# Optimization experiments

Hardware: AMD Instinct MI355X
Metric: run time of the kernel (lower is better)

Reference implementation:

```python
import jax, jax.numpy as jnp
import numpy as np

NH = 8          # attention heads
TOP_K = 2       # MoE top-k


def _ln(x, g, b, eps=1e-5):
    mu = x.mean(-1, keepdims=True)
    var = ((x - mu) ** 2).mean(-1, keepdims=True)
    return (x - mu) * jax.lax.rsqrt(var + eps) * g + b


def setup_inputs() -> dict:
    key = jax.random.key(0)
    ks = jax.random.split(key, 12)
    B, C, S, P, E, HID, NEXP, NCLS = 128, 3, 224, 16, 256, 1024, 6, 1000
    N = (S // P) ** 2
    def n(k, shape, scale=0.02):
        return scale * jax.random.normal(k, shape, jnp.float32)
    return dict(
        x=jax.random.normal(ks[0], (B, C, S, S), jnp.float32),
        conv_w=n(ks[1], (E, C, P, P)),
        conv_b=jnp.zeros((E,), jnp.float32),
        pos_embed=n(ks[2], (1, N, E)),
        ln1_g=jnp.ones((E,), jnp.float32), ln1_b=jnp.zeros((E,), jnp.float32),
        wqkv=n(ks[3], (3 * E, E)), bqkv=jnp.zeros((3 * E,), jnp.float32),
        wo=n(ks[4], (E, E)), bo=jnp.zeros((E,), jnp.float32),
        router_w=n(ks[5], (NEXP, E)), router_b=jnp.zeros((NEXP,), jnp.float32),
        w1=n(ks[6], (NEXP, E, HID)), b1=jnp.zeros((NEXP, HID), jnp.float32),
        w2=n(ks[7], (NEXP, HID, E)), b2=jnp.zeros((NEXP, E), jnp.float32),
        ln2_g=jnp.ones((E,), jnp.float32), ln2_b=jnp.zeros((E,), jnp.float32),
        head_w=n(ks[8], (NCLS, E)), head_b=jnp.zeros((NCLS,), jnp.float32),
    )


def reference(x, conv_w, conv_b, pos_embed, ln1_g, ln1_b, wqkv, bqkv, wo, bo,
              router_w, router_b, w1, b1, w2, b2, ln2_g, ln2_b, head_w, head_b):
    B, C, S, _ = x.shape
    E, _, P, _ = conv_w.shape
    G = S // P
    N = G * G
    hd = E // NH
    # --- patch embedding: strided conv == per-patch linear ---
    xr = x.reshape(B, C, G, P, G, P)
    tok = jnp.einsum('bchpwq,ecpq->bhwe', xr, conv_w).reshape(B, N, E) + conv_b
    tok = tok + pos_embed  # dropout is identity in eval
    # --- self-attention block (pre-norm, residual) ---
    xn = _ln(tok, ln1_g, ln1_b)
    qkv = xn @ wqkv.T + bqkv
    q, k, v = jnp.split(qkv, 3, axis=-1)
    q = q.reshape(B, N, NH, hd)
    k = k.reshape(B, N, NH, hd)
    v = v.reshape(B, N, NH, hd)
    scores = jnp.einsum('bqhd,bkhd->bhqk', q, k) / np.float32(np.sqrt(hd))
    attn = jax.nn.softmax(scores, axis=-1)
    ao = jnp.einsum('bhqk,bkhd->bqhd', attn, v).reshape(B, N, E)
    x1 = tok + ao @ wo.T + bo
    # --- MoE (top-k routing, eval: no noise) ---
    T = B * N
    flat = x1.reshape(T, E)
    probs = jax.nn.softmax(flat @ router_w.T + router_b, axis=-1)
    topw, topi = jax.lax.top_k(probs, TOP_K)  # [T,k]
    out = jnp.zeros_like(flat)
    n_experts = router_w.shape[0]
    for e in range(n_experts):  # fixed small expert loop
        gate = jnp.sum(jnp.where(topi == e, topw, 0.0), axis=-1)  # [T], 0 if unrouted
        h = jax.nn.gelu(flat @ w1[e] + b1[e], approximate=False)
        y = h @ w2[e] + b2[e]
        out = out + gate[:, None] * y
    # --- final norm, pool, head ---
    x2 = _ln(out.reshape(B, N, E), ln2_g, ln2_b)
    pooled = x2.mean(axis=1)
    return pooled @ head_w.T + head_b
```

## Files before the change

### kernel.cpp

```cpp
#include <hip/hip_runtime.h>
#include <hip/hip_bf16.h>

typedef unsigned short u16;
typedef short short8 __attribute__((ext_vector_type(8)));
typedef short short4v __attribute__((ext_vector_type(4)));
typedef float f32x4 __attribute__((ext_vector_type(4)));

#define T_TOK 25088
#define NTOK 196
#define SWZ(r, c) ((((((c) >> 3) ^ ((r) & 7)) << 3)) | ((c) & 7))
#define SWZ4(r, c) ((((((c) >> 2) & 16) | ((((c) >> 2) ^ (r)) & 15)) << 2) | ((c) & 3))

__device__ __forceinline__ u16 bfbits(float v) {
  __hip_bfloat16 h = __float2bfloat16(v);
  return *reinterpret_cast<u16*>(&h);
}
__device__ __forceinline__ float b2f(u16 u) {
  __hip_bfloat16 h = *reinterpret_cast<__hip_bfloat16*>(&u);
  return __bfloat162float(h);
}
__device__ __forceinline__ void fsplit(float v, u16& hi, u16& lo) {
  hi = bfbits(v);
  lo = bfbits(v - b2f(hi));
}

template<int EPI, bool SPLITA>
__global__ __launch_bounds__(256) void gemm_bs(
    const u16* __restrict__ A, const u16* __restrict__ Al,
    const u16* __restrict__ Bh, const u16* __restrict__ Bl,
    int M, int N, int K,
    const float* __restrict__ bias, const float* __restrict__ extra,
    float* __restrict__ outf, u16* __restrict__ obh)
{
  __shared__ u16 As[128][40];
  __shared__ u16 Asl[SPLITA ? 128 : 1][40];
  __shared__ u16 Bsh[128][40], Bsl[128][40];
  const int tid = threadIdx.x;
  const int lane = tid & 63, wave = tid >> 6;
  const int wm = wave >> 1, wn = wave & 1;
  const int row0 = blockIdx.x * 128, col0 = blockIdx.y * 128;

  const int r0 = tid >> 2, r1 = r0 + 64, co = (tid & 3) * 8;
  const int ar0 = row0 + r0, ar1 = row0 + r1;

  f32x4 acc[4][4];
  const f32x4 zero = {0.f, 0.f, 0.f, 0.f};
#pragma unroll
  for (int i = 0; i < 4; ++i)
#pragma unroll
    for (int j = 0; j < 4; ++j) acc[i][j] = zero;

  const int rsel = lane & 15, ksel = (lane >> 4) * 8;

  short8 ra, rl, rb0, rb1, rc0, rc1;
  auto issue = [&](int k0) {
    ra = *(const short8*)(A + (size_t)ar0 * K + k0 + co);
    rl = *(const short8*)(A + (size_t)ar1 * K + k0 + co);
    rb0 = *(const short8*)(Bh + (size_t)(col0 + r0) * K + k0 + co);
    rb1 = *(const short8*)(Bh + (size_t)(col0 + r1) * K + k0 + co);
    rc0 = *(const short8*)(Bl + (size_t)(col0 + r0) * K + k0 + co);
    rc1 = *(const short8*)(Bl + (size_t)(col0 + r1) * K + k0 + co);
  };
  short8 sa, sl;
  auto issueS = [&](int k0) {
    if constexpr (SPLITA) {
      sa = *(const short8*)(Al + (size_t)ar0 * K + k0 + co);
      sl = *(const short8*)(Al + (size_t)ar1 * K + k0 + co);
    }
  };
  auto commit = [&]() {
    *(short8*)&As[r0][co] = ra;
    *(short8*)&As[r1][co] = rl;
    if constexpr (SPLITA) {
      *(short8*)&Asl[r0][co] = sa;
      *(short8*)&Asl[r1][co] = sl;
    }
    *(short8*)&Bsh[r0][co] = rb0;
    *(short8*)&Bsh[r1][co] = rb1;
    *(short8*)&Bsl[r0][co] = rc0;
    *(short8*)&Bsl[r1][co] = rc1;
  };

  issue(0);
  issueS(0);
  commit();
  __syncthreads();

  for (int k0 = 0;;) {
    const bool more = (k0 + 32 < K);
    if (more) { issue(k0 + 32); issueS(k0 + 32); }
    short8 af[4], al4[4], bh4[4], bl4[4];
#pragma unroll
    for (int i = 0; i < 4; ++i) {
      af[i] = *(const short8*)&As[wm * 64 + i * 16 + rsel][ksel];
      if constexpr (SPLITA) al4[i] = *(const short8*)&Asl[wm * 64 + i * 16 + rsel][ksel];
    }
#pragma unroll
    for (int j = 0; j < 4; ++j) {
      bh4[j] = *(const short8*)&Bsh[wn * 64 + j * 16 + rsel][ksel];
      bl4[j] = *(const short8*)&Bsl[wn * 64 + j * 16 + rsel][ksel];
    }
#pragma unroll
    for (int i = 0; i < 4; ++i)
#pragma unroll
      for (int j = 0; j < 4; ++j) {
        acc[i][j] = __builtin_amdgcn_mfma_f32_16x16x32_bf16(af[i], bh4[j], acc[i][j], 0, 0, 0);
        if constexpr (SPLITA)
          acc[i][j] = __builtin_amdgcn_mfma_f32_16x16x32_bf16(al4[i], bh4[j], acc[i][j], 0, 0, 0);
        acc[i][j] = __builtin_amdgcn_mfma_f32_16x16x32_bf16(af[i], bl4[j], acc[i][j], 0, 0, 0);
      }
    k0 += 32;
    if (!more) break;
    __syncthreads();
    commit();
    __syncthreads();
  }

#pragma unroll
  for (int i = 0; i < 4; ++i) {
#pragma unroll
    for (int j = 0; j < 4; ++j) {
#pragma unroll
      for (int r = 0; r < 4; ++r) {
        int grow = row0 + wm * 64 + i * 16 + (lane >> 4) * 4 + r;
        int gcol = col0 + wn * 64 + j * 16 + rsel;
        float v = acc[i][j][r] + bias[gcol];
        size_t oi = (size_t)grow * N + gcol;
        if constexpr (EPI == 1) {
          v += extra[(size_t)(grow % NTOK) * N + gcol];
          outf[oi] = v;
        } else if constexpr (EPI == 2) {
          v += extra[oi];
          outf[oi] = v;
          obh[oi] = bfbits(v);
        } else if constexpr (EPI == 5) {
          obh[oi] = bfbits(v);
        }
      }
    }
  }
}

__global__ __launch_bounds__(512, 4) void moe_fused(
    const u16* __restrict__ x1h,
    const u16* __restrict__ w1, const u16* __restrict__ w2,
    const float* __restrict__ b1, const float* __restrict__ b2,
    const float* __restrict__ gates,
    const int* __restrict__ idx_all, const int* __restrict__ cnt_all,
    const int* __restrict__ base_all,
    float* __restrict__ yslot)
{
  const int e = blockIdx.z;
  const int Meff = cnt_all[e];
  const int row0 = blockIdx.x * 64;
  if (row0 >= Meff) return;
  const int* gidx = idx_all + (size_t)e * T_TOK;
  const int hbase = base_all[e];
  const u16* W1 = w1 + (size_t)e * 262144;
  const u16* W2 = w2 + (size_t)e * 262144;
  const float* B1 = b1 + e * 1024;
  const float* B2 = b2 + e * 256;

  __shared__ u16 Xs[64][256];
  __shared__ u16 Hs[64][128];
  __shared__ u16 Ws[2 * 128 * 64];

  const int tid = threadIdx.x, lane = tid & 63, wn = tid >> 6;
  const int rsel = lane & 15, ksel = (lane >> 4) * 8;
  const f32x4 zero = {0.f, 0.f, 0.f, 0.f};

  const int w1r = tid >> 2, w1c = ((2 * tid) & 7) * 8;
  const int w2r = tid >> 1, w2c = ((4 * tid) & 7) * 8;

  short8 w1a = *(const short8*)(W1 + (size_t)w1r * 256 + w1c);
  short8 w1b = *(const short8*)(W1 + (size_t)w1r * 256 + w1c + 8);
  for (int ch = tid; ch < 2048; ch += 512) {
    int r = ch >> 5, c = (ch & 31) * 8;
    int arr = gidx[min(row0 + r, Meff - 1)];
    *(short8*)&Xs[r][SWZ(r, c)] = *(const short8*)(x1h + (size_t)arr * 256 + c);
  }

  f32x4 acc2[2][4];
#pragma unroll
  for (int i = 0; i < 2; ++i)
#pragma unroll
    for (int j = 0; j < 4; ++j) acc2[i][j] = zero;

  f32x4 acc1[4];

  auto ph1 = [&](int st, int buf) {
#pragma unroll
    for (int kk = 0; kk < 2; ++kk) {
      int wrow = wn * 16 + rsel;
      int wc = kk * 32 + ksel;
      short8 wf = *(const short8*)&Ws[buf * 8192 + wrow * 64 + SWZ(wrow, wc)];
      int kglob = st * 64 + kk * 32 + ksel;
#pragma unroll
      for (int tt = 0; tt < 4; ++tt) {
        int xrow = tt * 16 + rsel;
        short8 xf = *(const short8*)&Xs[xrow][SWZ(xrow, kglob)];
        acc1[tt] = __builtin_amdgcn_mfma_f32_16x16x32_bf16(wf, xf, acc1[tt], 0, 0, 0);
      }
    }
  };
  auto ph2 = [&](int st) {
#pragma unroll
    for (int kk = 0; kk < 2; ++kk) {
      int wc = kk * 32 + ksel;
      short8 wf[2];
#pragma unroll
      for (int ot = 0; ot < 2; ++ot) {
        int wrow = wn * 32 + ot * 16 + rsel;
        wf[ot] = *(const short8*)&Ws[wrow * 64 + SWZ(wrow, wc)];
      }
      int kc = st * 64 + kk * 32 + ksel;
#pragma unroll
      for (int tt = 0; tt < 4; ++tt) {
        int tok = tt * 16 + rsel;
        short4v lo = *(const short4v*)&Hs[tok][SWZ4(tok, kc)];
        short4v hi = *(const short4v*)&Hs[tok][SWZ4(tok, kc + 4)];
        short8 hf = {lo[0], lo[1], lo[2], lo[3], hi[0], hi[1], hi[2], hi[3]};
#pragma unroll
        for (int ot = 0; ot < 2; ++ot)
          acc2[ot][tt] = __builtin_amdgcn_mfma_f32_16x16x32_bf16(wf[ot], hf, acc2[ot][tt], 0, 0, 0);
      }
    }
  };

  for (int hc = 0; hc < 8; ++hc) {
    const u16* W1c = W1 + (size_t)hc * 128 * 256;
    const u16* W2c = W2 + hc * 128;
    short8 q0 = *(const short8*)(W2c + (size_t)w2r * 1024 + w2c);
    short8 q1 = *(const short8*)(W2c + (size_t)w2r * 1024 + w2c + 8);
    short8 q2 = *(const short8*)(W2c + (size_t)w2r * 1024 + w2c + 16);
    short8 q3 = *(const short8*)(W2c + (size_t)w2r * 1024 + w2c + 24);

#pragma unroll
    for (int i = 0; i < 4; ++i) acc1[i] = zero;

    *(short8*)&Ws[w1r * 64 + SWZ(w1r, w1c)] = w1a;
    *(short8*)&Ws[w1r * 64 + SWZ(w1r, w1c + 8)] = w1b;
    short8 p0 = *(const short8*)(W1c + (size_t)w1r * 256 + 64 + w1c);
    short8 p1 = *(const short8*)(W1c + (size_t)w1r * 256 + 64 + w1c + 8);
    __syncthreads();
    short8 s0 = *(const short8*)(W1c + (size_t)w1r * 256 + 128 + w1c);
    short8 s1 = *(const short8*)(W1c + (size_t)w1r * 256 + 128 + w1c + 8);
    ph1(0, 0);
    *(short8*)&Ws[8192 + w1r * 64 + SWZ(w1r, w1c)] = p0;
    *(short8*)&Ws[8192 + w1r * 64 + SWZ(w1r, w1c + 8)] = p1;
    __syncthreads();
    p0 = *(const short8*)(W1c + (size_t)w1r * 256 + 192 + w1c);
    p1 = *(const short8*)(W1c + (size_t)w1r * 256 + 192 + w1c + 8);
    ph1(1, 1);
    *(short8*)&Ws[w1r * 64 + SWZ(w1r, w1c)] = s0;
    *(short8*)&Ws[w1r * 64 + SWZ(w1r, w1c + 8)] = s1;
    __syncthreads();
    ph1(2, 0);
    *(short8*)&Ws[8192 + w1r * 64 + SWZ(w1r, w1c)] = p0;
    *(short8*)&Ws[8192 + w1r * 64 + SWZ(w1r, w1c + 8)] = p1;
    __syncthreads();
    ph1(3, 1);

#pragma unroll
    for (int tt = 0; tt < 4; ++tt) {
      int tok = tt * 16 + rsel;
      int hid0 = wn * 16 + (lane >> 4) * 4;
      u16 hv[4];
#pragma unroll
      for (int r = 0; r < 4; ++r) {
        float v = acc1[tt][r] + B1[hc * 128 + hid0 + r];
        float u = 1.5957691216057308f * (v + 0.044715f * v * v * v);
        hv[r] = bfbits(v / (1.f + __expf(-u)));
      }
      *(ushort4*)&Hs[tok][SWZ4(tok, hid0)] = make_ushort4(hv[0], hv[1], hv[2], hv[3]);
    }
    __syncthreads();

    *(short8*)&Ws[w2r * 64 + SWZ(w2r, w2c)] = q0;
    *(short8*)&Ws[w2r * 64 + SWZ(w2r, w2c + 8)] = q1;
    *(short8*)&Ws[w2r * 64 + SWZ(w2r, w2c + 16)] = q2;
    *(short8*)&Ws[w2r * 64 + SWZ(w2r, w2c + 24)] = q3;
    q0 = *(const short8*)(W2c + (size_t)w2r * 1024 + 64 + w2c);
    q1 = *(const short8*)(W2c + (size_t)w2r * 1024 + 64 + w2c + 8);
    q2 = *(const short8*)(W2c + (size_t)w2r * 1024 + 64 + w2c + 16);
    q3 = *(const short8*)(W2c + (size_t)w2r * 1024 + 64 + w2c + 24);
    __syncthreads();
    ph2(0);
    __syncthreads();
    *(short8*)&Ws[w2r * 64 + SWZ(w2r, w2c)] = q0;
    *(short8*)&Ws[w2r * 64 + SWZ(w2r, w2c + 8)] = q1;
    *(short8*)&Ws[w2r * 64 + SWZ(w2r, w2c + 16)] = q2;
    *(short8*)&Ws[w2r * 64 + SWZ(w2r, w2c + 24)] = q3;
    if (hc < 7) {
      w1a = *(const short8*)(W1 + (size_t)((hc + 1) * 128 + w1r) * 256 + w1c);
      w1b = *(const short8*)(W1 + (size_t)((hc + 1) * 128 + w1r) * 256 + w1c + 8);
    }
    __syncthreads();
    ph2(1);
    __syncthreads();
  }

#pragma unroll
  for (int tt = 0; tt < 4; ++tt) {
    int grow = row0 + tt * 16 + rsel;
    if (grow < Meff) {
      int tk = gidx[grow];
      float gt = gates[(size_t)tk * 6 + e];
#pragma unroll
      for (int ot = 0; ot < 2; ++ot) {
        int out0 = wn * 32 + ot * 16 + (lane >> 4) * 4;
        float4 w4 = make_float4(gt * (acc2[ot][tt][0] + B2[out0]),
                                gt * (acc2[ot][tt][1] + B2[out0 + 1]),
                                gt * (acc2[ot][tt][2] + B2[out0 + 2]),
                                gt * (acc2[ot][tt][3] + B2[out0 + 3]));
        *(float4*)&yslot[(size_t)(hbase + grow) * 256 + out0] = w4;
      }
    }
  }
}

__global__ void im2col_split(const float* __restrict__ x,
                             u16* __restrict__ Aph, u16* __restrict__ Apl) {
  int id = blockIdx.x * 256 + threadIdx.x;
  if (id >= T_TOK * 192) return;
  int t = id / 192, kk = id - t * 192;
  int k4 = kk * 4;
  int c = k4 >> 8, rem = k4 & 255, p = rem >> 4, q = rem & 15;
  int b = t / 196, n = t - b * 196, gh = n / 14, gw = n - gh * 14;
  const float4 v = *(const float4*)(x + ((size_t)(b * 3 + c) * 224 + gh * 16 + p) * 224 + gw * 16 + q);
  u16 h0, l0, h1, l1, h2, l2, h3, l3;
  fsplit(v.x, h0, l0); fsplit(v.y, h1, l1); fsplit(v.z, h2, l2); fsplit(v.w, h3, l3);
  *(ushort4*)(Aph + (size_t)t * 768 + k4) = make_ushort4(h0, h1, h2, h3);
  *(ushort4*)(Apl + (size_t)t * 768 + k4) = make_ushort4(l0, l1, l2, l3);
}

__global__ __launch_bounds__(256) void ln_kernel(const float* __restrict__ in,
    const float* __restrict__ g, const float* __restrict__ b, u16* __restrict__ oh)
{
  const int lane = threadIdx.x & 63;
  const int t = blockIdx.x * 4 + (threadIdx.x >> 6);
  const float4 v = *(const float4*)(in + (size_t)t * 256 + lane * 4);
  float s = v.x + v.y + v.z + v.w;
  float sq = v.x * v.x + v.y * v.y + v.z * v.z + v.w * v.w;
#pragma unroll
  for (int o = 32; o >= 1; o >>= 1) {
    s  += __shfl_xor(s,  o, 64);
    sq += __shfl_xor(sq, o, 64);
  }
  float mu = s * (1.f / 256.f);
  float var = sq * (1.f / 256.f) - mu * mu;
  float rstd = rsqrtf(var + 1e-5f);
  const float4 gv = *(const float4*)(g + lane * 4);
  const float4 bv = *(const float4*)(b + lane * 4);
  *(ushort4*)(oh + (size_t)t * 256 + lane * 4) = make_ushort4(
      bfbits((v.x - mu) * rstd * gv.x + bv.x), bfbits((v.y - mu) * rstd * gv.y + bv.y),
      bfbits((v.z - mu) * rstd * gv.z + bv.z), bfbits((v.w - mu) * rstd * gv.w + bv.w));
}

__global__ __launch_bounds__(256) void ln2_combine(const float* __restrict__ yslot,
    const int* __restrict__ invslot,
    const float* __restrict__ g, const float* __restrict__ b, float* __restrict__ outf)
{
  const int lane = threadIdx.x & 63;
  const int t = blockIdx.x * 4 + (threadIdx.x >> 6);
  const int s0 = invslot[t * 2], s1 = invslot[t * 2 + 1];
  const float4 a = *(const float4*)(yslot + (size_t)s0 * 256 + lane * 4);
  const float4 c = *(const float4*)(yslot + (size_t)s1 * 256 + lane * 4);
  float4 v = make_float4(a.x + c.x, a.y + c.y, a.z + c.z, a.w + c.w);
  float s = v.x + v.y + v.z + v.w;
  float sq = v.x * v.x + v.y * v.y + v.z * v.z + v.w * v.w;
#pragma unroll
  for (int o = 32; o >= 1; o >>= 1) {
    s  += __shfl_xor(s,  o, 64);
    sq += __shfl_xor(sq, o, 64);
  }
  float mu = s * (1.f / 256.f);
  float var = sq * (1.f / 256.f) - mu * mu;
  float rstd = rsqrtf(var + 1e-5f);
  const float4 gv = *(const float4*)(g + lane * 4);
  const float4 bv = *(const float4*)(b + lane * 4);
  *(float4*)(outf + (size_t)t * 256 + lane * 4) = make_float4(
      (v.x - mu) * rstd * gv.x + bv.x, (v.y - mu) * rstd * gv.y + bv.y,
      (v.z - mu) * rstd * gv.z + bv.z, (v.w - mu) * rstd * gv.w + bv.w);
}

__global__ __launch_bounds__(256) void attn_mfma(const u16* __restrict__ qkvb,
                                                 u16* __restrict__ aoh, u16* __restrict__ aol) {
  __shared__ u16 Qs[208][40];
  __shared__ u16 Ks[208][40];
  __shared__ u16 Vt[32][256];
  __shared__ u16 Ps[4][16][232];
  const int tid = threadIdx.x, lane = tid & 63, wave = tid >> 6;
  const int b = blockIdx.x >> 3, h = blockIdx.x & 7;
  const size_t base = (size_t)b * 196 * 768 + h * 32;
  const short8 z8 = {0, 0, 0, 0, 0, 0, 0, 0};

  for (int idx = tid; idx < 832; idx += 256) {
    int r = idx >> 2, c = (idx & 3) * 8;
    short8 q = z8, k = z8;
    if (r < 196) {
      q = *(const short8*)(qkvb + base + (size_t)r * 768 + c);
      k = *(const short8*)(qkvb + base + (size_t)r * 768 + 256 + c);
    }
    *(short8*)&Qs[r][c] = q;
    *(short8*)&Ks[r][c] = k;
  }
  for (int idx = tid; idx < 32 * 224; idx += 256) {
    int c = idx & 31, k = idx >> 5;
    u16 v = 0;
    if (k < 196) v = qkvb[base + (size_t)k * 768 + 512 + c];
    Vt[c][k ^ ((c & 7) << 3)] = v;
  }
  {
    int r = lane >> 2, c0 = 208 + (lane & 3) * 4;
    Ps[wave][r][c0] = 0; Ps[wave][r][c0 + 1] = 0; Ps[wave][r][c0 + 2] = 0; Ps[wave][r][c0 + 3] = 0;
  }
  __syncthreads();

  const int rsel = lane & 15, ksel = (lane >> 4) * 8;
  const f32x4 zero = {0.f, 0.f, 0.f, 0.f};

  for (int mt = wave; mt < 13; mt += 4) {
    short8 aq = *(const short8*)&Qs[mt * 16 + rsel][ksel];
    f32x4 sacc[13];
#pragma unroll
    for (int n = 0; n < 13; ++n)
      sacc[n] = __builtin_amdgcn_mfma_f32_16x16x32_bf16(
          aq, *(const short8*)&Ks[n * 16 + rsel][ksel], zero, 0, 0, 0);

#pragma unroll
    for (int r = 0; r < 4; ++r) {
      float mv = -1e30f;
#pragma unroll
      for (int n = 0; n < 13; ++n) {
        float sv = sacc[n][r] * 0.17677669529663687f;
        sacc[n][r] = sv;
        if (n * 16 + rsel < 196) mv = fmaxf(mv, sv);
      }
      mv = fmaxf(mv, __shfl_xor(mv, 1, 64));
      mv = fmaxf(mv, __shfl_xor(mv, 2, 64));
      mv = fmaxf(mv, __shfl_xor(mv, 4, 64));
      mv = fmaxf(mv, __shfl_xor(mv, 8, 64));
      float sm = 0.f;
#pragma unroll
      for (int n = 0; n < 13; ++n) {
        float p = (n * 16 + rsel < 196) ? __expf(sacc[n][r] - mv) : 0.f;
        sacc[n][r] = p;
        sm += p;
      }
      sm += __shfl_xor(sm, 1, 64);
      sm += __shfl_xor(sm, 2, 64);
      sm += __shfl_xor(sm, 4, 64);
      sm += __shfl_xor(sm, 8, 64);
      float inv = 1.f / sm;
      int prow = (lane >> 4) * 4 + r;
#pragma unroll
      for (int n = 0; n < 13; ++n)
        Ps[wave][prow][n * 16 + rsel] = bfbits(sacc[n][r] * inv);
    }

    f32x4 oacc[2] = {zero, zero};
#pragma unroll
    for (int kk = 0; kk < 7; ++kk) {
      short8 ap = *(const short8*)&Ps[wave][rsel][kk * 32 + ksel];
#pragma unroll
      for (int nt = 0; nt < 2; ++nt) {
        int d = nt * 16 + rsel;
        short8 bv = *(const short8*)&Vt[d][(kk * 32 + ksel) ^ ((d & 7) << 3)];
        oacc[nt] = __builtin_amdgcn_mfma_f32_16x16x32_bf16(ap, bv, oacc[nt], 0, 0, 0);
      }
    }
#pragma unroll
    for (int nt = 0; nt < 2; ++nt) {
#pragma unroll
      for (int r = 0; r < 4; ++r) {
        int row = mt * 16 + (lane >> 4) * 4 + r;
        if (row < 196) {
          size_t oi = ((size_t)b * 196 + row) * 256 + h * 32 + nt * 16 + rsel;
          u16 hh, ll; fsplit(oacc[nt][r], hh, ll);
          aoh[oi] = hh; aol[oi] = ll;
        }
      }
    }
  }
}

__global__ __launch_bounds__(256) void router_kernel(const float* __restrict__ x1,
    const float* __restrict__ rw, const float* __restrict__ rb, float* __restrict__ gates)
{
  const int lane = threadIdx.x & 63;
  const int t = blockIdx.x * 4 + (threadIdx.x >> 6);
  const float4 xv = *(const float4*)(x1 + (size_t)t * 256 + lane * 4);
  float logit[6];
#pragma unroll
  for (int e = 0; e < 6; ++e) {
    const float4 wv = *(const float4*)(rw + e * 256 + lane * 4);
    float p = xv.x * wv.x + xv.y * wv.y + xv.z * wv.z + xv.w * wv.w;
#pragma unroll
    for (int o = 32; o >= 1; o >>= 1) p += __shfl_xor(p, o, 64);
    logit[e] = p + rb[e];
  }
  float mx = logit[0];
#pragma unroll
  for (int e = 1; e < 6; ++e) mx = fmaxf(mx, logit[e]);
  float pe[6], sum = 0.f;
#pragma unroll
  for (int e = 0; e < 6; ++e) { pe[e] = __expf(logit[e] - mx); sum += pe[e]; }
  float inv = 1.f / sum;
  int i1 = 0; float p1 = pe[0];
#pragma unroll
  for (int e = 1; e < 6; ++e) if (pe[e] > p1) { p1 = pe[e]; i1 = e; }
  int i2 = -1; float p2 = -1.f;
#pragma unroll
  for (int e = 0; e < 6; ++e) if (e != i1 && pe[e] > p2) { p2 = pe[e]; i2 = e; }
  if (lane < 6)
    gates[(size_t)t * 6 + lane] = (lane == i1) ? p1 * inv : ((lane == i2) ? p2 * inv : 0.f);
}

__global__ __launch_bounds__(256) void scatter_kernel(const float* __restrict__ gates,
                                                      int* __restrict__ cnt, int* __restrict__ idx) {
  __shared__ int lcnt[6], lbase[6];
  const int t = blockIdx.x * 256 + threadIdx.x;
  if (threadIdx.x < 6) lcnt[threadIdx.x] = 0;
  __syncthreads();
  float g[6]; int lpos[6];
#pragma unroll
  for (int e = 0; e < 6; ++e) {
    g[e] = gates[(size_t)t * 6 + e];
    if (g[e] > 0.f) lpos[e] = atomicAdd(&lcnt[e], 1);
  }
  __syncthreads();
  if (threadIdx.x < 6) lbase[threadIdx.x] = atomicAdd(&cnt[threadIdx.x], lcnt[threadIdx.x]);
  __syncthreads();
#pragma unroll
  for (int e = 0; e < 6; ++e)
    if (g[e] > 0.f) idx[(size_t)e * T_TOK + lbase[e] + lpos[e]] = t;
}

__global__ void prefix6_kernel(const int* __restrict__ cnt, int* __restrict__ base) {
  if (threadIdx.x == 0) {
    int s = 0;
#pragma unroll
    for (int e = 0; e < 6; ++e) { base[e] = s; s += cnt[e]; }
  }
}

__global__ __launch_bounds__(256) void slotmap_kernel(const int* __restrict__ idx,
    const int* __restrict__ cnt, const int* __restrict__ base,
    int* __restrict__ nslot, int* __restrict__ invslot) {
  const int e = blockIdx.y;
  const int p = blockIdx.x * 256 + threadIdx.x;
  if (p < cnt[e]) {
    int t = idx[(size_t)e * T_TOK + p];
    int j = atomicAdd(&nslot[t], 1);
    invslot[(size_t)t * 2 + j] = base[e] + p;
  }
}

__global__ __launch_bounds__(256) void pool_kernel(const float* __restrict__ x2, float* __restrict__ pooled) {
  int b = blockIdx.x, e = threadIdx.x;
  float s = 0.f;
  for (int n = 0; n < 196; ++n) s += x2[((size_t)b * 196 + n) * 256 + e];
  pooled[(size_t)b * 256 + e] = s * (1.f / 196.f);
}

__global__ __launch_bounds__(256) void head_kernel(const float* __restrict__ pooled,
    const float* __restrict__ hw, const float* __restrict__ hb, float* __restrict__ out) {
  __shared__ float p[256];
  int b = blockIdx.x;
  p[threadIdx.x] = pooled[(size_t)b * 256 + threadIdx.x];
  __syncthreads();
  for (int cls = threadIdx.x; cls < 1000; cls += 256) {
    const float* w = hw + (size_t)cls * 256;
    float s = hb[cls];
    for (int k = 0; k < 256; k += 4)
      s += p[k] * w[k] + p[k + 1] * w[k + 1] + p[k + 2] * w[k + 2] + p[k + 3] * w[k + 3];
    out[(size_t)b * 1000 + cls] = s;
  }
}

__global__ void cast_split_kernel(const float* __restrict__ in,
                                  u16* __restrict__ oh, u16* __restrict__ ol, int n4) {
  int id = blockIdx.x * 256 + threadIdx.x;
  if (id >= n4) return;
  float4 v = ((const float4*)in)[id];
  u16 h0, l0, h1, l1, h2, l2, h3, l3;
  fsplit(v.x, h0, l0); fsplit(v.y, h1, l1); fsplit(v.z, h2, l2); fsplit(v.w, h3, l3);
  ((ushort4*)oh)[id] = make_ushort4(h0, h1, h2, h3);
  ((ushort4*)ol)[id] = make_ushort4(l0, l1, l2, l3);
}

__global__ __launch_bounds__(256) void transpose_cast(const float* __restrict__ in,
    u16* __restrict__ oh, int R, int C) {
  __shared__ float tile[32][33];
  const int e = blockIdx.z;
  const int bc = blockIdx.x * 32, br = blockIdx.y * 32;
  const int tx = threadIdx.x & 31, ty = threadIdx.x >> 5;
  const float* src = in + (size_t)e * R * C;
#pragma unroll
  for (int i = 0; i < 32; i += 8)
    tile[ty + i][tx] = src[(size_t)(br + ty + i) * C + bc + tx];
  __syncthreads();
#pragma unroll
  for (int i = 0; i < 32; i += 8) {
    size_t di = (size_t)e * R * C + (size_t)(bc + ty + i) * R + br + tx;
    oh[di] = bfbits(tile[tx][ty + i]);
  }
}

extern "C" void kernel_launch(void* const* d_in, const int* in_sizes, int n_in,
                              void* d_out, int out_size, void* d_ws, size_t ws_size,
                              hipStream_t stream) {
  (void)in_sizes; (void)n_in; (void)out_size; (void)ws_size;
  const float* x      = (const float*)d_in[0];
  const float* conv_w = (const float*)d_in[1];
  const float* conv_b = (const float*)d_in[2];
  const float* pos    = (const float*)d_in[3];
  const float* ln1_g  = (const float*)d_in[4];
  const float* ln1_b  = (const float*)d_in[5];
  const float* wqkv   = (const float*)d_in[6];
  const float* bqkv   = (const float*)d_in[7];
  const float* wo     = (const float*)d_in[8];
  const float* bo     = (const float*)d_in[9];
  const float* rw     = (const float*)d_in[10];
  const float* rb     = (const float*)d_in[11];
  const float* w1     = (const float*)d_in[12];
  const float* b1     = (const float*)d_in[13];
  const float* w2     = (const float*)d_in[14];
  const float* b2     = (const float*)d_in[15];
  const float* ln2_g  = (const float*)d_in[16];
  const float* ln2_b  = (const float*)d_in[17];
  const float* hw     = (const float*)d_in[18];
  const float* hb     = (const float*)d_in[19];
  float* out = (float*)d_out;

  const int T = T_TOK;
  char* ws = (char*)d_ws;
  size_t off = 0;
  auto alloc = [&](size_t bytes) -> void* {
    void* p = ws + off;
    off += (bytes + 255) & ~(size_t)255;
    return p;
  };
  u16*   Aph    = (u16*)  alloc((size_t)T * 768 * 2);
  u16*   Apl    = (u16*)  alloc((size_t)T * 768 * 2);
  float* tok    = (float*)alloc((size_t)T * 256 * 4);
  u16*   xnh    = (u16*)  alloc((size_t)T * 256 * 2);
  u16*   qkvb   = (u16*)  alloc((size_t)T * 768 * 2);
  u16*   aoh    = (u16*)  alloc((size_t)T * 256 * 2);
  u16*   aol    = (u16*)  alloc((size_t)T * 256 * 2);
  float* x1f    = (float*)alloc((size_t)T * 256 * 4);
  u16*   x1h    = (u16*)  alloc((size_t)T * 256 * 2);
  float* gates  = (float*)alloc((size_t)T * 6 * 4);
  int*   idx    = (int*)  alloc((size_t)6 * T * 4);
  int*   cnt    = (int*)  alloc(256);
  int*   base   = (int*)  alloc(256);
  int*   nslot  = (int*)  alloc((size_t)T * 4);
  int*   invslot= (int*)  alloc((size_t)2 * T * 4);
  float* pooled = (float*)alloc((size_t)128 * 256 * 4);
  u16*   cwh    = (u16*)  alloc((size_t)196608 * 2);
  u16*   cwl    = (u16*)  alloc((size_t)196608 * 2);
  u16*   wqh    = (u16*)  alloc((size_t)196608 * 2);
  u16*   wql    = (u16*)  alloc((size_t)196608 * 2);
  u16*   woh    = (u16*)  alloc((size_t)65536 * 2);
  u16*   wol    = (u16*)  alloc((size_t)65536 * 2);
  u16*   w1th   = (u16*)  alloc((size_t)6 * 262144 * 2);
  u16*   w2th   = (u16*)  alloc((size_t)6 * 262144 * 2);
  float* yslot = (float*)aoh;
  float* x2    = (float*)ws;

  cast_split_kernel<<<192, 256, 0, stream>>>(conv_w, cwh, cwl, 49152);
  cast_split_kernel<<<192, 256, 0, stream>>>(wqkv, wqh, wql, 49152);
  cast_split_kernel<<<64, 256, 0, stream>>>(wo, woh, wol, 16384);
  transpose_cast<<<dim3(32, 8, 6), 256, 0, stream>>>(w1, w1th, 256, 1024);
  transpose_cast<<<dim3(8, 32, 6), 256, 0, stream>>>(w2, w2th, 1024, 256);

  im2col_split<<<18816, 256, 0, stream>>>(x, Aph, Apl);
  gemm_bs<1, true><<<dim3(196, 2), 256, 0, stream>>>(Aph, Apl, cwh, cwl, T, 256, 768,
      conv_b, pos, tok, nullptr);

  ln_kernel<<<6272, 256, 0, stream>>>(tok, ln1_g, ln1_b, xnh);
  gemm_bs<5, false><<<dim3(196, 6), 256, 0, stream>>>(xnh, nullptr, wqh, wql, T, 768, 256,
      bqkv, nullptr, nullptr, qkvb);
  attn_mfma<<<1024, 256, 0, stream>>>(qkvb, aoh, aol);
  gemm_bs<2, true><<<dim3(196, 2), 256, 0, stream>>>(aoh, aol, woh, wol, T, 256, 256,
      bo, tok, x1f, x1h);

  router_kernel<<<6272, 256, 0, stream>>>(x1f, rw, rb, gates);
  hipMemsetAsync(cnt, 0, 256, stream);
  scatter_kernel<<<98, 256, 0, stream>>>(gates, cnt, idx);
  prefix6_kernel<<<1, 64, 0, stream>>>(cnt, base);
  hipMemsetAsync(nslot, 0, (size_t)T * 4, stream);
  slotmap_kernel<<<dim3(98, 6), 256, 0, stream>>>(idx, cnt, base, nslot, invslot);
  moe_fused<<<dim3(392, 1, 6), 512, 0, stream>>>(x1h, w1th, w2th,
      b1, b2, gates, idx, cnt, base, yslot);

  ln2_combine<<<6272, 256, 0, stream>>>(yslot, invslot, ln2_g, ln2_b, x2);
  pool_kernel<<<128, 256, 0, stream>>>(x2, pooled);
  head_kernel<<<128, 256, 0, stream>>>(pooled, hw, hb, out);
}
```

Measured before the change: 421.8 us.

## Fuse im2col and bf16 hi/lo split into the patch-embedding GEMM

Removes the separate im2col_split kernel and its two bf16 intermediate buffers. The new patch GEMM reads fp32 pixels straight from the image, splits them into hi/lo bf16 in registers and writes them to shared memory. This avoids writing and re-reading about 77 MB of intermediates. The trade-off is that the A-tile loads become strided image reads and the split arithmetic is repeated for each column block, since the grid has two column blocks.

```diff
diff --git a/kernel.cpp b/kernel.cpp
--- a/kernel.cpp
+++ b/kernel.cpp
@@ -126,16 +126,131 @@
         int gcol = col0 + wn * 64 + j * 16 + rsel;
         float v = acc[i][j][r] + bias[gcol];
         size_t oi = (size_t)grow * N + gcol;
-        if constexpr (EPI == 1) {
-          v += extra[(size_t)(grow % NTOK) * N + gcol];
-          outf[oi] = v;
-        } else if constexpr (EPI == 2) {
+        if constexpr (EPI == 2) {
           v += extra[oi];
           outf[oi] = v;
           obh[oi] = bfbits(v);
         } else if constexpr (EPI == 5) {
           obh[oi] = bfbits(v);
         }
+      }
+    }
+  }
+}
+
+__global__ __launch_bounds__(256) void gemm_patch(
+    const float* __restrict__ xin,
+    const u16* __restrict__ Bh, const u16* __restrict__ Bl,
+    const float* __restrict__ bias, const float* __restrict__ pos,
+    float* __restrict__ outf)
+{
+  __shared__ u16 As[128][40], Asl[128][40];
+  __shared__ u16 Bsh[128][40], Bsl[128][40];
+  const int tid = threadIdx.x;
+  const int lane = tid & 63, wave = tid >> 6;
+  const int wm = wave >> 1, wn = wave & 1;
+  const int row0 = blockIdx.x * 128, col0 = blockIdx.y * 128;
+  const int rsel = lane & 15, ksel = (lane >> 4) * 8;
+  const int K = 768, N = 256;
+
+  const int ar = tid >> 1, ph = tid & 1;
+  const float* srcbase;
+  {
+    int t = row0 + ar;
+    int b = t / 196, n = t - b * 196;
+    int gh = n / 14, gw = n - gh * 14;
+    srcbase = xin + ((size_t)(b * 3) * 224 + gh * 16) * 224 + gw * 16;
+  }
+  const int br0 = tid >> 2, br1 = br0 + 64, bco = (tid & 3) * 8;
+
+  f32x4 acc[4][4];
+  const f32x4 zero = {0.f, 0.f, 0.f, 0.f};
+#pragma unroll
+  for (int i = 0; i < 4; ++i)
+#pragma unroll
+    for (int j = 0; j < 4; ++j) acc[i][j] = zero;
+
+  float4 fa0, fa1, fa2, fa3;
+  short8 rb0, rb1, rc0, rc1;
+  auto issue = [&](int k0) {
+    int c = k0 >> 8, p = ((k0 >> 4) & 15) + ph;
+    const float* s = srcbase + ((size_t)c * 224 + p) * 224;
+    fa0 = *(const float4*)(s);
+    fa1 = *(const float4*)(s + 4);
+    fa2 = *(const float4*)(s + 8);
+    fa3 = *(const float4*)(s + 12);
+    rb0 = *(const short8*)(Bh + (size_t)(col0 + br0) * K + k0 + bco);
+    rb1 = *(const short8*)(Bh + (size_t)(col0 + br1) * K + k0 + bco);
+    rc0 = *(const short8*)(Bl + (size_t)(col0 + br0) * K + k0 + bco);
+    rc1 = *(const short8*)(Bl + (size_t)(col0 + br1) * K + k0 + bco);
+  };
+  auto commit = [&]() {
+    float f[16] = {fa0.x, fa0.y, fa0.z, fa0.w, fa1.x, fa1.y, fa1.z, fa1.w,
+                   fa2.x, fa2.y, fa2.z, fa2.w, fa3.x, fa3.y, fa3.z, fa3.w};
+    u16 hv[16], lv[16];
+#pragma unroll
+    for (int j = 0; j < 16; ++j) fsplit(f[j], hv[j], lv[j]);
+    short8 h0 = {(short)hv[0], (short)hv[1], (short)hv[2], (short)hv[3],
+                 (short)hv[4], (short)hv[5], (short)hv[6], (short)hv[7]};
+    short8 h1 = {(short)hv[8], (short)hv[9], (short)hv[10], (short)hv[11],
+                 (short)hv[12], (short)hv[13], (short)hv[14], (short)hv[15]};
+    short8 l0 = {(short)lv[0], (short)lv[1], (short)lv[2], (short)lv[3],
+                 (short)lv[4], (short)lv[5], (short)lv[6], (short)lv[7]};
+    short8 l1 = {(short)lv[8], (short)lv[9], (short)lv[10], (short)lv[11],
+                 (short)lv[12], (short)lv[13], (short)lv[14], (short)lv[15]};
+    *(short8*)&As[ar][ph * 16] = h0;
+    *(short8*)&As[ar][ph * 16 + 8] = h1;
+    *(short8*)&Asl[ar][ph * 16] = l0;
+    *(short8*)&Asl[ar][ph * 16 + 8] = l1;
+    *(short8*)&Bsh[br0][bco] = rb0;
+    *(short8*)&Bsh[br1][bco] = rb1;
+    *(short8*)&Bsl[br0][bco] = rc0;
+    *(short8*)&Bsl[br1][bco] = rc1;
+  };
+
+  issue(0);
+  commit();
+  __syncthreads();
+
+  for (int k0 = 0;;) {
+    const bool more = (k0 + 32 < K);
+    if (more) issue(k0 + 32);
+    short8 af[4], al4[4], bh4[4], bl4[4];
+#pragma unroll
+    for (int i = 0; i < 4; ++i) {
+      af[i] = *(const short8*)&As[wm * 64 + i * 16 + rsel][ksel];
+      al4[i] = *(const short8*)&Asl[wm * 64 + i * 16 + rsel][ksel];
+    }
+#pragma unroll
+    for (int j = 0; j < 4; ++j) {
+      bh4[j] = *(const short8*)&Bsh[wn * 64 + j * 16 + rsel][ksel];
+      bl4[j] = *(const short8*)&Bsl[wn * 64 + j * 16 + rsel][ksel];
+    }
+#pragma unroll
+    for (int i = 0; i < 4; ++i)
+#pragma unroll
+      for (int j = 0; j < 4; ++j) {
+        acc[i][j] = __builtin_amdgcn_mfma_f32_16x16x32_bf16(af[i], bh4[j], acc[i][j], 0, 0, 0);
+        acc[i][j] = __builtin_amdgcn_mfma_f32_16x16x32_bf16(al4[i], bh4[j], acc[i][j], 0, 0, 0);
+        acc[i][j] = __builtin_amdgcn_mfma_f32_16x16x32_bf16(af[i], bl4[j], acc[i][j], 0, 0, 0);
+      }
+    k0 += 32;
+    if (!more) break;
+    __syncthreads();
+    commit();
+    __syncthreads();
+  }
+
+#pragma unroll
+  for (int i = 0; i < 4; ++i) {
+#pragma unroll
+    for (int j = 0; j < 4; ++j) {
+#pragma unroll
+      for (int r = 0; r < 4; ++r) {
+        int grow = row0 + wm * 64 + i * 16 + (lane >> 4) * 4 + r;
+        int gcol = col0 + wn * 64 + j * 16 + rsel;
+        float v = acc[i][j][r] + bias[gcol] + pos[(size_t)(grow % NTOK) * N + gcol];
+        outf[(size_t)grow * N + gcol] = v;
       }
     }
   }
@@ -317,21 +432,6 @@
       }
     }
   }
-}
-
-__global__ void im2col_split(const float* __restrict__ x,
-                             u16* __restrict__ Aph, u16* __restrict__ Apl) {
-  int id = blockIdx.x * 256 + threadIdx.x;
-  if (id >= T_TOK * 192) return;
-  int t = id / 192, kk = id - t * 192;
-  int k4 = kk * 4;
-  int c = k4 >> 8, rem = k4 & 255, p = rem >> 4, q = rem & 15;
-  int b = t / 196, n = t - b * 196, gh = n / 14, gw = n - gh * 14;
-  const float4 v = *(const float4*)(x + ((size_t)(b * 3 + c) * 224 + gh * 16 + p) * 224 + gw * 16 + q);
-  u16 h0, l0, h1, l1, h2, l2, h3, l3;
-  fsplit(v.x, h0, l0); fsplit(v.y, h1, l1); fsplit(v.z, h2, l2); fsplit(v.w, h3, l3);
-  *(ushort4*)(Aph + (size_t)t * 768 + k4) = make_ushort4(h0, h1, h2, h3);
-  *(ushort4*)(Apl + (size_t)t * 768 + k4) = make_ushort4(l0, l1, l2, l3);
 }
 
 __global__ __launch_bounds__(256) void ln_kernel(const float* __restrict__ in,
@@ -642,8 +742,6 @@
     off += (bytes + 255) & ~(size_t)255;
     return p;
   };
-  u16*   Aph    = (u16*)  alloc((size_t)T * 768 * 2);
-  u16*   Apl    = (u16*)  alloc((size_t)T * 768 * 2);
   float* tok    = (float*)alloc((size_t)T * 256 * 4);
   u16*   xnh    = (u16*)  alloc((size_t)T * 256 * 2);
   u16*   qkvb   = (u16*)  alloc((size_t)T * 768 * 2);
@@ -675,9 +773,7 @@
   transpose_cast<<<dim3(32, 8, 6), 256, 0, stream>>>(w1, w1th, 256, 1024);
   transpose_cast<<<dim3(8, 32, 6), 256, 0, stream>>>(w2, w2th, 1024, 256);
 
-  im2col_split<<<18816, 256, 0, stream>>>(x, Aph, Apl);
-  gemm_bs<1, true><<<dim3(196, 2), 256, 0, stream>>>(Aph, Apl, cwh, cwl, T, 256, 768,
-      conv_b, pos, tok, nullptr);
+  gemm_patch<<<dim3(196, 2), 256, 0, stream>>>(x, cwh, cwl, conv_b, pos, tok);
 
   ln_kernel<<<6272, 256, 0, stream>>>(tok, ln1_g, ln1_b, xnh);
   gemm_bs<5, false><<<dim3(196, 6), 256, 0, stream>>>(xnh, nullptr, wqh, wql, T, 768, 256,
```

New measurement: 391.8 us (median of 2 runs). 7.1% less time.
